# Optimization experiments

Hardware: AMD Instinct MI355X
Metric: run time of the kernel (lower is better)

Reference implementation:

```python
import jax, jax.numpy as jnp
import numpy as np

# Mamba2 config derived from __init__ defaults
D_MODEL, D_STATE, D_CONV, EXPAND, HEADDIM = 768, 16, 4, 2, 64
D_INNER = EXPAND * D_MODEL                      # 1536
NHEADS = D_INNER // HEADDIM                     # 24
NGROUPS = 1
CONV_DIM = D_INNER + 2 * NGROUPS * D_STATE      # 1568
D_IN_PROJ = 2 * D_INNER + 2 * NGROUPS * D_STATE + NHEADS  # 3128
EPS = 1e-5


def setup_inputs() -> dict:
    key = jax.random.key(0)
    ks = jax.random.split(key, 8)
    B, L = 2, 4096
    x = jax.random.normal(ks[0], (B, L, D_MODEL), jnp.float32)
    s_in = 1.0 / np.sqrt(D_MODEL)
    s_out = 1.0 / np.sqrt(D_INNER)
    W_in = jax.random.uniform(ks[1], (D_IN_PROJ, D_MODEL), jnp.float32, -s_in, s_in)
    W_out = jax.random.uniform(ks[2], (D_MODEL, D_INNER), jnp.float32, -s_out, s_out)
    conv_w = jax.random.uniform(ks[3], (CONV_DIM, D_CONV), jnp.float32, -0.5, 0.5)
    conv_b = jax.random.uniform(ks[4], (CONV_DIM,), jnp.float32, -0.5, 0.5)
    # dt init in [1e-3, 0.1] (log-uniform), stored as inverse-softplus bias
    dt = jnp.exp(jax.random.uniform(ks[5], (NHEADS,), jnp.float32) * (np.log(0.1) - np.log(1e-3)) + np.log(1e-3))
    dt_bias = dt + jnp.log(-jnp.expm1(-dt))
    A_log = jnp.log(jax.random.uniform(ks[6], (NHEADS,), jnp.float32, 1.0, 16.0))
    D = jnp.ones((NHEADS,), jnp.float32)
    ln_w = jnp.ones((D_MODEL,), jnp.float32)
    ln_b = jnp.zeros((D_MODEL,), jnp.float32)
    gate_norm_w = jnp.ones((D_INNER,), jnp.float32)
    return dict(x=x, ln_w=ln_w, ln_b=ln_b, W_in=W_in, conv_w=conv_w, conv_b=conv_b,
                dt_bias=dt_bias, A_log=A_log, D=D, gate_norm_w=gate_norm_w, W_out=W_out)


def _layernorm(x, w, b):
    mu = x.mean(-1, keepdims=True)
    var = ((x - mu) ** 2).mean(-1, keepdims=True)
    return (x - mu) * jax.lax.rsqrt(var + EPS) * w + b


def _silu(x):
    return x * jax.nn.sigmoid(x)


def _mamba_block(x, ln_w, ln_b, W_in, conv_w, conv_b, dt_bias, A_log, D, gate_norm_w, W_out):
    Bsz, L, _ = x.shape
    u = _layernorm(x, ln_w, ln_b)
    zxbcdt = jnp.einsum('bld,ed->ble', u, W_in)                 # (b,l,3128)
    z = zxbcdt[..., :D_INNER]
    xBC = zxbcdt[..., D_INNER:D_INNER + CONV_DIM]
    dt = jax.nn.softplus(zxbcdt[..., -NHEADS:] + dt_bias)       # (b,l,h)
    # causal depthwise conv (width D_CONV) + SiLU
    xp = jnp.pad(xBC, ((0, 0), (D_CONV - 1, 0), (0, 0)))
    acc = xp[:, 0:L, :] * conv_w[:, 0]
    for i in range(1, D_CONV):
        acc = acc + xp[:, i:i + L, :] * conv_w[:, i]
    xBC = _silu(acc + conv_b)
    xs = xBC[..., :D_INNER].reshape(Bsz, L, NHEADS, HEADDIM)    # (b,l,h,p)
    Bm = xBC[..., D_INNER:D_INNER + D_STATE]                    # (b,l,n) ngroups=1
    Cm = xBC[..., D_INNER + D_STATE:]                           # (b,l,n)
    A = -jnp.exp(A_log)                                         # (h,)
    dA = jnp.exp(dt * A)                                        # (b,l,h)
    # selective scan: h_t = dA_t * h_{t-1} + dt_t * (x_t outer B_t)
    def step(h, inp):
        dA_t, dt_t, B_t, C_t, x_t = inp                          # (b,h),(b,h),(b,n),(b,n),(b,h,p)
        h = dA_t[..., None, None] * h + jnp.einsum('bh,bn,bhp->bhpn', dt_t, B_t, x_t)
        y = jnp.einsum('bhpn,bn->bhp', h, C_t)
        return h, y
    h0 = jnp.zeros((Bsz, NHEADS, HEADDIM, D_STATE), x.dtype)
    _, ys = jax.lax.scan(step, h0, (dA.transpose(1, 0, 2), dt.transpose(1, 0, 2),
                                    Bm.transpose(1, 0, 2), Cm.transpose(1, 0, 2),
                                    xs.transpose(1, 0, 2, 3)))
    y = ys.transpose(1, 0, 2, 3) + D[:, None] * xs               # (b,l,h,p) skip term
    y = y.reshape(Bsz, L, D_INNER)
    # gated RMSNorm: norm(y * silu(z)) * weight
    g = y * _silu(z)
    g = g * jax.lax.rsqrt((g * g).mean(-1, keepdims=True) + EPS) * gate_norm_w
    out = jnp.einsum('ble,de->bld', g, W_out)
    return x + out


def reference(x, ln_w, ln_b, W_in, conv_w, conv_b, dt_bias, A_log, D, gate_norm_w, W_out):
    return _mamba_block(x, ln_w, ln_b, W_in, conv_w, conv_b, dt_bias, A_log, D, gate_norm_w, W_out)
```

## Files before the change

### kernel.cpp

```cpp
#include <hip/hip_runtime.h>
#include <hip/hip_bf16.h>
#include <stdint.h>

#define SEQ      4096
#define BATCH    2
#define NTOK     (BATCH*SEQ)
#define DMODEL   768
#define DINNER   1536
#define NHEADS   24
#define HEADDIM  64
#define DSTATE   16
#define NPAD     3200
#define EPSV     1e-5f
#define CHUNK    64
#define NCHUNK   (SEQ/CHUNK)
#define SUB      32

typedef __bf16 bf16x8 __attribute__((ext_vector_type(8)));
typedef float  floatx4 __attribute__((ext_vector_type(4)));

__device__ __forceinline__ unsigned short f2bf(float f) {
    union { float f; uint32_t u; } v; v.f = f;
    uint32_t u = v.u;
    uint32_t r = (u + 0x7fffu + ((u >> 16) & 1u)) >> 16;
    return (unsigned short)r;
}

__device__ __forceinline__ float bf2f(unsigned short h) {
    union { uint32_t u; float f; } v; v.u = (uint32_t)h << 16;
    return v.f;
}

__device__ __forceinline__ float bfl(uint32_t u) {
    union { uint32_t u; float f; } v; v.u = u << 16; return v.f;
}
__device__ __forceinline__ float bfh(uint32_t u) {
    union { uint32_t u; float f; } v; v.u = u & 0xffff0000u; return v.f;
}
__device__ __forceinline__ uint32_t packbf(float lo, float hi) {
    return (uint32_t)f2bf(lo) | ((uint32_t)f2bf(hi) << 16);
}

__device__ __forceinline__ float siluf(float x) { return x / (1.f + __expf(-x)); }

__device__ __forceinline__ void async_cp16(const void* g, void* l) {
    __builtin_amdgcn_global_load_lds(
        (const __attribute__((address_space(1))) void*)g,
        (__attribute__((address_space(3))) void*)l,
        16, 0, 0);
}

__global__ __launch_bounds__(256) void cvt_kernel(
    const float* __restrict__ Win, const float* __restrict__ Wout,
    unsigned short* __restrict__ win16, unsigned short* __restrict__ wout16)
{
    int idx = blockIdx.x * 256 + threadIdx.x;
    const int n1 = NPAD * DMODEL;
    if (idx < n1) {
        int r = idx / DMODEL;
        win16[idx] = (r < 3128) ? f2bf(Win[idx]) : (unsigned short)0;
    } else {
        int i2 = idx - n1;
        if (i2 < DMODEL * DINNER) wout16[i2] = f2bf(Wout[i2]);
    }
}

__global__ __launch_bounds__(256) void ln_kernel(
    const float* __restrict__ x, const float* __restrict__ lnw, const float* __restrict__ lnb,
    unsigned short* __restrict__ u16)
{
    int wave = threadIdx.x >> 6, lane = threadIdx.x & 63;
    int token = blockIdx.x * 4 + wave;
    const float* row = x + (size_t)token * DMODEL;
    float4 v[3];
    float s = 0.f, ss = 0.f;
#pragma unroll
    for (int j = 0; j < 3; ++j) {
        v[j] = *(const float4*)(row + lane*4 + j*256);
        s  += v[j].x + v[j].y + v[j].z + v[j].w;
        ss += v[j].x*v[j].x + v[j].y*v[j].y + v[j].z*v[j].z + v[j].w*v[j].w;
    }
#pragma unroll
    for (int o = 32; o > 0; o >>= 1) { s += __shfl_xor(s, o, 64); ss += __shfl_xor(ss, o, 64); }
    float mean = s * (1.f/768.f);
    float var  = ss * (1.f/768.f) - mean*mean;
    float rstd = rsqrtf(var + EPSV);
    unsigned short* brow = u16 + (size_t)token * DMODEL;
#pragma unroll
    for (int j = 0; j < 3; ++j) {
        int cidx = lane*4 + j*256;
        float4 w4 = *(const float4*)(lnw + cidx);
        float4 b4 = *(const float4*)(lnb + cidx);
        float a0 = (v[j].x - mean)*rstd*w4.x + b4.x;
        float a1 = (v[j].y - mean)*rstd*w4.y + b4.y;
        float a2 = (v[j].z - mean)*rstd*w4.z + b4.z;
        float a3 = (v[j].w - mean)*rstd*w4.w + b4.w;
        ushort4 p; p.x = f2bf(a0); p.y = f2bf(a1); p.z = f2bf(a2); p.w = f2bf(a3);
        *(ushort4*)(brow + cidx) = p;
    }
}

__global__ __launch_bounds__(256) void dt_kernel(
    const float* __restrict__ raw24, const float* __restrict__ dt_bias,
    const float* __restrict__ A_log, float* __restrict__ dtT, float* __restrict__ dAT)
{
    int tid = blockIdx.x * 256 + threadIdx.x;
    int h   = tid >> 13;
    int tok = tid & (NTOK-1);
    float raw = raw24[(size_t)tok*NHEADS + h] + dt_bias[h];
    float dt = (raw > 20.f) ? raw : log1pf(__expf(raw));
    float A = -__expf(A_log[h]);
    dtT[tid] = dt;
    dAT[tid] = __expf(dt * A);
}

__global__ __launch_bounds__(256, 3) void gemm1_kernel(
    const unsigned short* __restrict__ A, const unsigned short* __restrict__ Bt,
    unsigned short* __restrict__ z16, unsigned short* __restrict__ x16,
    float* __restrict__ bcr, float* __restrict__ raw24)
{
    constexpr int K = DMODEL;
    __shared__ unsigned short As[128*64];
    __shared__ unsigned short Bs[128*64];
    const int tid  = threadIdx.x;
    const int lane = tid & 63;
    const int wave = tid >> 6;
    const int id   = blockIdx.x;
    const int xcd  = id & 7;
    const int j5   = id >> 3;
    const int m0 = (xcd*8 + (j5 & 7)) * 128;
    const int n0 = (j5 >> 3) * 128;
    const int wm = (wave & 1) * 64;
    const int wn = (wave >> 1) * 64;

    floatx4 acc[4][4];
#pragma unroll
    for (int i = 0; i < 4; ++i)
#pragma unroll
        for (int j = 0; j < 4; ++j) acc[i][j] = floatx4{0.f, 0.f, 0.f, 0.f};

    const int srow8  = lane >> 3;
    const int schunk = lane & 7;
    const int sscol  = (schunk ^ srow8) * 8;

    for (int k0 = 0; k0 < K; k0 += 64) {
        __syncthreads();
#pragma unroll
        for (int o = 0; o < 4; ++o) {
            int row = wave*32 + o*8 + srow8;
            async_cp16(A + (size_t)(m0 + row) * K + k0 + sscol, As + row*64 + schunk*8);
        }
#pragma unroll
        for (int o = 0; o < 4; ++o) {
            int row = wave*32 + o*8 + srow8;
            async_cp16(Bt + (size_t)(n0 + row) * K + k0 + sscol, Bs + row*64 + schunk*8);
        }
        __syncthreads();
        const int fr  = lane & 15;
        const int q8  = lane >> 4;
        const int key = fr & 7;
#pragma unroll
        for (int ks = 0; ks < 2; ++ks) {
            const int ch = ((ks*4 + q8) ^ key) * 8;
            bf16x8 a[4], b[4];
#pragma unroll
            for (int i = 0; i < 4; ++i)
                a[i] = *(const bf16x8*)(As + (wm + i*16 + fr)*64 + ch);
#pragma unroll
            for (int j = 0; j < 4; ++j)
                b[j] = *(const bf16x8*)(Bs + (wn + j*16 + fr)*64 + ch);
#pragma unroll
            for (int i = 0; i < 4; ++i)
#pragma unroll
                for (int j = 0; j < 4; ++j)
                    acc[i][j] = __builtin_amdgcn_mfma_f32_16x16x32_bf16(a[i], b[j], acc[i][j], 0, 0, 0);
        }
    }

    const int col = lane & 15;
    const int rq  = (lane >> 4) * 4;
    if (n0 < DINNER) {
#pragma unroll
        for (int i = 0; i < 4; ++i)
#pragma unroll
            for (int j = 0; j < 4; ++j)
#pragma unroll
                for (int r = 0; r < 4; ++r) {
                    int gm = m0 + wm + i*16 + rq + r;
                    int gn = n0 + wn + j*16 + col;
                    z16[(size_t)gm * DINNER + gn] = f2bf(acc[i][j][r]);
                }
    } else if (n0 < 3072) {
#pragma unroll
        for (int i = 0; i < 4; ++i)
#pragma unroll
            for (int j = 0; j < 4; ++j)
#pragma unroll
                for (int r = 0; r < 4; ++r) {
                    int gm = m0 + wm + i*16 + rq + r;
                    int gn = n0 + wn + j*16 + col;
                    x16[(size_t)gm * DINNER + (gn - DINNER)] = f2bf(acc[i][j][r]);
                }
    } else {
#pragma unroll
        for (int i = 0; i < 4; ++i)
#pragma unroll
            for (int j = 0; j < 4; ++j)
#pragma unroll
                for (int r = 0; r < 4; ++r) {
                    int gm = m0 + wm + i*16 + rq + r;
                    int gn = n0 + wn + j*16 + col;
                    if (gn < 3104)
                        bcr[(size_t)gm * 32 + (gn - 3072)] = acc[i][j][r];
                    else if (gn < 3128)
                        raw24[(size_t)gm * NHEADS + (gn - 3104)] = acc[i][j][r];
                }
    }
}

__global__ __launch_bounds__(256, 4) void gemm2_kernel(
    const unsigned short* __restrict__ A, const unsigned short* __restrict__ Bt,
    float* __restrict__ Cf, const float* __restrict__ resid)
{
    constexpr int K = DINNER;
    __shared__ unsigned short As[64*64];
    __shared__ unsigned short Bs[128*64];
    const int tid  = threadIdx.x;
    const int lane = tid & 63;
    const int wave = tid >> 6;
    const int id   = blockIdx.x;
    const int xcd  = id & 7;
    const int j6   = id >> 3;
    const int m0 = (xcd*16 + j6/6) * 64;
    const int n0 = (j6 % 6) * 128;
    const int wm = (wave & 1) * 32;
    const int wn = (wave >> 1) * 64;

    floatx4 acc[2][4];
#pragma unroll
    for (int i = 0; i < 2; ++i)
#pragma unroll
        for (int j = 0; j < 4; ++j) acc[i][j] = floatx4{0.f, 0.f, 0.f, 0.f};

    const int srow8  = lane >> 3;
    const int schunk = lane & 7;
    const int sscol  = (schunk ^ srow8) * 8;

    for (int k0 = 0; k0 < K; k0 += 64) {
        __syncthreads();
#pragma unroll
        for (int o = 0; o < 2; ++o) {
            int row = wave*16 + o*8 + srow8;
            async_cp16(A + (size_t)(m0 + row) * K + k0 + sscol, As + row*64 + schunk*8);
        }
#pragma unroll
        for (int o = 0; o < 4; ++o) {
            int row = wave*32 + o*8 + srow8;
            async_cp16(Bt + (size_t)(n0 + row) * K + k0 + sscol, Bs + row*64 + schunk*8);
        }
        __syncthreads();
        const int fr  = lane & 15;
        const int q8  = lane >> 4;
        const int key = fr & 7;
#pragma unroll
        for (int ks = 0; ks < 2; ++ks) {
            const int ch = ((ks*4 + q8) ^ key) * 8;
            bf16x8 a[2], b[4];
#pragma unroll
            for (int i = 0; i < 2; ++i)
                a[i] = *(const bf16x8*)(As + (wm + i*16 + fr)*64 + ch);
#pragma unroll
            for (int j = 0; j < 4; ++j)
                b[j] = *(const bf16x8*)(Bs + (wn + j*16 + fr)*64 + ch);
#pragma unroll
            for (int i = 0; i < 2; ++i)
#pragma unroll
                for (int j = 0; j < 4; ++j)
                    acc[i][j] = __builtin_amdgcn_mfma_f32_16x16x32_bf16(a[i], b[j], acc[i][j], 0, 0, 0);
        }
    }

    const int col = lane & 15;
    const int rq  = (lane >> 4) * 4;
#pragma unroll
    for (int i = 0; i < 2; ++i)
#pragma unroll
        for (int j = 0; j < 4; ++j)
#pragma unroll
            for (int r = 0; r < 4; ++r) {
                int gm = m0 + wm + i*16 + rq + r;
                int gn = n0 + wn + j*16 + col;
                Cf[(size_t)gm * DMODEL + gn] = acc[i][j][r] + resid[(size_t)gm * DMODEL + gn];
            }
}

__global__ __launch_bounds__(256) void scan_pass1(
    const unsigned short* __restrict__ x16, const float* __restrict__ bcr,
    const float* __restrict__ dAT, const float* __restrict__ dtT,
    const float* __restrict__ cw, const float* __restrict__ cb, const float* __restrict__ Dp,
    float* __restrict__ hloc, float* __restrict__ pprod, unsigned short* __restrict__ ylocal16)
{
    int wave = threadIdx.x >> 6, lane = threadIdx.x & 63;
    int blk = blockIdx.x * 4 + wave;
    int c = blk & (NCHUNK-1), bh = blk >> 6;
    int h = bh % NHEADS, b = bh / NHEADS;
    int row0 = b * SEQ + c * CHUNK;
    int l0 = c * CHUNK;
    int tb = h * NTOK + row0;
    __shared__ float bcraw[4][35][32];
    __shared__ float bcsc[4][32][32];
    __shared__ float av[4][32], dv[4][32];

    const int cx = h*64 + lane;
    float cwx0 = cw[cx*4+0], cwx1 = cw[cx*4+1], cwx2 = cw[cx*4+2], cwx3 = cw[cx*4+3];
    float cbx = cb[cx];
    const int nBC = lane & 31;
    float cwc0 = cw[(DINNER+nBC)*4+0], cwc1 = cw[(DINNER+nBC)*4+1];
    float cwc2 = cw[(DINNER+nBC)*4+2], cwc3 = cw[(DINNER+nBC)*4+3];
    float cbc = cb[DINNER+nBC];
    float Dh = Dp[h];

    float xm3 = (l0 >= 3) ? bf2f(x16[(size_t)(row0-3)*DINNER + cx]) : 0.f;
    float xm2 = (l0 >= 2) ? bf2f(x16[(size_t)(row0-2)*DINNER + cx]) : 0.f;
    float xm1 = (l0 >= 1) ? bf2f(x16[(size_t)(row0-1)*DINNER + cx]) : 0.f;

    float hst[16];
#pragma unroll
    for (int n = 0; n < 16; ++n) hst[n] = 0.f;
    float aprod = 1.f;

    for (int sc = 0; sc < CHUNK/SUB; ++sc) {
        int rb = row0 + sc * SUB;
        int lb = l0 + sc * SUB;
        __syncthreads();
#pragma unroll
        for (int it = 0; it < 5; ++it) {
            int idx = it*64 + lane;
            if (idx < 280) {
                int s = idx >> 3, q = idx & 7;
                float4 val = {0.f,0.f,0.f,0.f};
                if (lb - 3 + s >= 0)
                    val = *(const float4*)(bcr + (size_t)(rb-3+s)*32 + q*4);
                *(float4*)&bcraw[wave][s][q*4] = val;
            }
        }
        if (lane < 32) av[wave][lane] = dAT[(size_t)tb + sc*SUB + lane];
        else           dv[wave][lane-32] = dtT[(size_t)tb + sc*SUB + lane - 32];
        float xr[SUB];
#pragma unroll
        for (int s = 0; s < SUB; ++s)
            xr[s] = bf2f(x16[(size_t)(rb+s)*DINNER + cx]);
        __syncthreads();
#pragma unroll
        for (int it = 0; it < 16; ++it) {
            int s = it*2 + (lane >> 5);
            float v = cbc + bcraw[wave][s][nBC]*cwc0 + bcraw[wave][s+1][nBC]*cwc1
                          + bcraw[wave][s+2][nBC]*cwc2 + bcraw[wave][s+3][nBC]*cwc3;
            bcsc[wave][s][nBC] = siluf(v);
        }
        __syncthreads();
#pragma unroll 2
        for (int s = 0; s < SUB; ++s) {
            float a = av[wave][s];
            float xc = siluf(cbx + xm3*cwx0 + xm2*cwx1 + xm1*cwx2 + xr[s]*cwx3);
            xm3 = xm2; xm2 = xm1; xm1 = xr[s];
            float scale = dv[wave][s] * xc;
            float y = Dh * xc;
            const float4* bp4 = (const float4*)&bcsc[wave][s][0];
            float4 bv[8];
#pragma unroll
            for (int q = 0; q < 8; ++q) bv[q] = bp4[q];
            const float* bp = (const float*)bv;
#pragma unroll
            for (int n = 0; n < 16; ++n) hst[n] = a*hst[n] + scale*bp[n];
#pragma unroll
            for (int n = 0; n < 16; ++n) y += hst[n] * bp[16+n];
            aprod *= a;
            ylocal16[(size_t)(rb+s)*DINNER + cx] = f2bf(y);
        }
    }
    float* o = hloc + (size_t)blk * 1024 + lane * 16;
#pragma unroll
    for (int n = 0; n < 16; ++n) o[n] = hst[n];
    if (lane == 0) pprod[blk] = aprod;
}

__global__ __launch_bounds__(256) void scan_pass2(
    const float* __restrict__ hloc, const float* __restrict__ pprod, float* __restrict__ hstart)
{
    __shared__ float sm[64*256];
    __shared__ float pp[64];
    const int tid = threadIdx.x;
    const int bh  = blockIdx.x >> 2;
    const int q   = blockIdx.x & 3;
    const float* src = hloc + (size_t)bh * 65536 + q * 256;
#pragma unroll
    for (int it = 0; it < 16; ++it) {
        int idx = it*256 + tid;
        int c   = idx >> 6;
        int e4  = (idx & 63) * 4;
        *(float4*)&sm[c*256 + e4] = *(const float4*)(src + (size_t)c*1024 + e4);
    }
    if (tid < 64) pp[tid] = pprod[bh*64 + tid];
    __syncthreads();
    float h = 0.f;
    float* dst = hstart + (size_t)bh * 65536 + q * 256 + tid;
#pragma unroll 8
    for (int c = 0; c < 64; ++c) {
        dst[(size_t)c * 1024] = h;
        h = pp[c] * h + sm[c*256 + tid];
    }
}

__global__ __launch_bounds__(256) void scan_pass3(
    const float* __restrict__ bcr, const float* __restrict__ dAT,
    const float* __restrict__ cw, const float* __restrict__ cb,
    const float* __restrict__ hstart, unsigned short* __restrict__ ylocal16)
{
    int wave = threadIdx.x >> 6, lane = threadIdx.x & 63;
    int blk = blockIdx.x * 4 + wave;
    int c = blk & (NCHUNK-1), bh = blk >> 6;
    int h = bh % NHEADS, b = bh / NHEADS;
    int row0 = b * SEQ + c * CHUNK;
    int l0 = c * CHUNK;
    int tb = h * NTOK + row0;
    __shared__ float craw[4][35][16];
    __shared__ float csc[4][32][16];
    __shared__ float av[4][32];

    const int cx = h*64 + lane;
    const int nC = lane & 15;
    float cwc0 = cw[(DINNER+16+nC)*4+0], cwc1 = cw[(DINNER+16+nC)*4+1];
    float cwc2 = cw[(DINNER+16+nC)*4+2], cwc3 = cw[(DINNER+16+nC)*4+3];
    float cbc = cb[DINNER+16+nC];

    float h0[16];
    const float* hs = hstart + (size_t)blk * 1024 + lane * 16;
#pragma unroll
    for (int n = 0; n < 16; ++n) h0[n] = hs[n];
    float cd = 1.f;

    for (int sc = 0; sc < CHUNK/SUB; ++sc) {
        int rb = row0 + sc * SUB;
        int lb = l0 + sc * SUB;
        __syncthreads();
#pragma unroll
        for (int it = 0; it < 3; ++it) {
            int idx = it*64 + lane;
            if (idx < 140) {
                int s = idx >> 2, q = idx & 3;
                float4 val = {0.f,0.f,0.f,0.f};
                if (lb - 3 + s >= 0)
                    val = *(const float4*)(bcr + (size_t)(rb-3+s)*32 + 16 + q*4);
                *(float4*)&craw[wave][s][q*4] = val;
            }
        }
        if (lane < 32) av[wave][lane] = dAT[(size_t)tb + sc*SUB + lane];
        float yr[SUB];
#pragma unroll
        for (int s = 0; s < SUB; ++s)
            yr[s] = bf2f(ylocal16[(size_t)(rb+s)*DINNER + cx]);
        __syncthreads();
#pragma unroll
        for (int it = 0; it < 8; ++it) {
            int s = it*4 + (lane >> 4);
            float v = cbc + craw[wave][s][nC]*cwc0 + craw[wave][s+1][nC]*cwc1
                          + craw[wave][s+2][nC]*cwc2 + craw[wave][s+3][nC]*cwc3;
            csc[wave][s][nC] = siluf(v);
        }
        __syncthreads();
#pragma unroll 2
        for (int s = 0; s < SUB; ++s) {
            cd *= av[wave][s];
            const float4* cp4 = (const float4*)&csc[wave][s][0];
            float4 cv[4];
#pragma unroll
            for (int q = 0; q < 4; ++q) cv[q] = cp4[q];
            const float* cp = (const float*)cv;
            float corr = 0.f;
#pragma unroll
            for (int n = 0; n < 16; ++n) corr += cp[n] * h0[n];
            ylocal16[(size_t)(rb+s)*DINNER + cx] = f2bf(yr[s] + cd * corr);
        }
    }
}

__global__ __launch_bounds__(256) void gate_kernel(
    const unsigned short* __restrict__ yv16, const unsigned short* __restrict__ z16,
    const float* __restrict__ gw, unsigned short* __restrict__ g16)
{
    int wave = threadIdx.x >> 6, lane = threadIdx.x & 63;
    int token = blockIdx.x * 4 + wave;
    const uint4* yrow = (const uint4*)(yv16 + (size_t)token * DINNER);
    const uint4* zrow = (const uint4*)(z16 + (size_t)token * DINNER);
    float g[3][8];
    float ss = 0.f;
#pragma unroll
    for (int j = 0; j < 3; ++j) {
        uint4 y8 = yrow[lane + j*64];
        uint4 z8 = zrow[lane + j*64];
        const uint32_t* yp = (const uint32_t*)&y8;
        const uint32_t* zp = (const uint32_t*)&z8;
#pragma unroll
        for (int q = 0; q < 4; ++q) {
            float a = bfl(yp[q]) * siluf(bfl(zp[q]));
            float bvl = bfh(yp[q]) * siluf(bfh(zp[q]));
            g[j][q*2]   = a;
            g[j][q*2+1] = bvl;
            ss += a*a + bvl*bvl;
        }
    }
#pragma unroll
    for (int o = 32; o > 0; o >>= 1) ss += __shfl_xor(ss, o, 64);
    float scale = rsqrtf(ss * (1.f/1536.f) + EPSV);
    uint4* orow = (uint4*)(g16 + (size_t)token * DINNER);
#pragma unroll
    for (int j = 0; j < 3; ++j) {
        int ebase = (lane + j*64) * 8;
        float4 w0 = *(const float4*)(gw + ebase);
        float4 w1 = *(const float4*)(gw + ebase + 4);
        uint4 p;
        p.x = packbf(g[j][0]*scale*w0.x, g[j][1]*scale*w0.y);
        p.y = packbf(g[j][2]*scale*w0.z, g[j][3]*scale*w0.w);
        p.z = packbf(g[j][4]*scale*w1.x, g[j][5]*scale*w1.y);
        p.w = packbf(g[j][6]*scale*w1.z, g[j][7]*scale*w1.w);
        orow[lane + j*64] = p;
    }
}

extern "C" void kernel_launch(void* const* d_in, const int* in_sizes, int n_in,
                              void* d_out, int out_size, void* d_ws, size_t ws_size,
                              hipStream_t stream)
{
    const float* x        = (const float*)d_in[0];
    const float* ln_w     = (const float*)d_in[1];
    const float* ln_b     = (const float*)d_in[2];
    const float* W_in     = (const float*)d_in[3];
    const float* conv_w   = (const float*)d_in[4];
    const float* conv_b   = (const float*)d_in[5];
    const float* dt_bias  = (const float*)d_in[6];
    const float* A_log    = (const float*)d_in[7];
    const float* Dp       = (const float*)d_in[8];
    const float* gate_w   = (const float*)d_in[9];
    const float* W_out    = (const float*)d_in[10];
    float* out = (float*)d_out;

    char* ws = (char*)d_ws;
    size_t off = 0;
    auto alloc = [&](size_t bytes) -> void* {
        void* p = ws + off;
        off += (bytes + 255) & ~(size_t)255;
        return p;
    };
    unsigned short* u16    = (unsigned short*)alloc((size_t)NTOK*DMODEL*2);
    unsigned short* win16  = (unsigned short*)alloc((size_t)NPAD*DMODEL*2);
    float*          dtT    = (float*)alloc((size_t)NTOK*NHEADS*4);
    float*          dAT    = (float*)alloc((size_t)NTOK*NHEADS*4);
    float*          raw24  = (float*)alloc((size_t)NTOK*NHEADS*4);
    unsigned short* x16    = (unsigned short*)alloc((size_t)NTOK*DINNER*2);
    float*          bcr    = (float*)alloc((size_t)NTOK*32*4);
    unsigned short* wout16 = (unsigned short*)alloc((size_t)DMODEL*DINNER*2);
    unsigned short* z16    = (unsigned short*)alloc((size_t)NTOK*DINNER*2);
    unsigned short* y16    = (unsigned short*)alloc((size_t)NTOK*DINNER*2);
    unsigned short* g16    = (unsigned short*)alloc((size_t)NTOK*DINNER*2);
    float*          pprod  = (float*)alloc((size_t)BATCH*NHEADS*NCHUNK*4);
    float* hloc   = (float*)u16;
    float* hstart = (float*)g16;

    cvt_kernel<<<(NPAD*DMODEL + DMODEL*DINNER)/256, 256, 0, stream>>>(W_in, W_out, win16, wout16);
    ln_kernel<<<NTOK/4, 256, 0, stream>>>(x, ln_w, ln_b, u16);
    gemm1_kernel<<<1600, 256, 0, stream>>>(u16, win16, z16, x16, bcr, raw24);
    dt_kernel<<<NTOK*NHEADS/256, 256, 0, stream>>>(raw24, dt_bias, A_log, dtT, dAT);
    scan_pass1<<<BATCH*NHEADS*NCHUNK/4, 256, 0, stream>>>(x16, bcr, dAT, dtT, conv_w, conv_b, Dp, hloc, pprod, y16);
    scan_pass2<<<BATCH*NHEADS*4, 256, 0, stream>>>(hloc, pprod, hstart);
    scan_pass3<<<BATCH*NHEADS*NCHUNK/4, 256, 0, stream>>>(bcr, dAT, conv_w, conv_b, hstart, y16);
    gate_kernel<<<NTOK/4, 256, 0, stream>>>(y16, z16, gate_w, g16);
    gemm2_kernel<<<768, 256, 0, stream>>>(g16, wout16, out, x);
}
```

Measured before the change: 261.8 us.

## Fuse LN with weight conversion, fold dt into GEMM1 epilogue, enlarge GEMM2 tile

Merges the layernorm and weight-conversion kernels into one prep launch and vectorizes the fp32-to-bf16 conversion to four elements per thread. Moves the softplus/exp dt computation into the GEMM1 epilogue, which removes the raw24 buffer and a separate kernel. Switches GEMM2 from 64x128 to 128x128 tiles with 384 blocks. This cuts launches and memory round trips. The trade-off is lower occupancy and fewer blocks in GEMM2, plus strided transposed stores from the GEMM1 epilogue.

```diff
diff --git a/kernel.cpp b/kernel.cpp
--- a/kernel.cpp
+++ b/kernel.cpp
@@ -15,6 +15,7 @@
 #define CHUNK    64
 #define NCHUNK   (SEQ/CHUNK)
 #define SUB      32
+#define LNBLK    2048
 
 typedef __bf16 bf16x8 __attribute__((ext_vector_type(8)));
 typedef float  floatx4 __attribute__((ext_vector_type(4)));
@@ -50,74 +51,70 @@
         16, 0, 0);
 }
 
-__global__ __launch_bounds__(256) void cvt_kernel(
+__global__ __launch_bounds__(256) void prep_kernel(
+    const float* __restrict__ x, const float* __restrict__ lnw, const float* __restrict__ lnb,
+    unsigned short* __restrict__ u16,
     const float* __restrict__ Win, const float* __restrict__ Wout,
     unsigned short* __restrict__ win16, unsigned short* __restrict__ wout16)
 {
-    int idx = blockIdx.x * 256 + threadIdx.x;
-    const int n1 = NPAD * DMODEL;
-    if (idx < n1) {
-        int r = idx / DMODEL;
-        win16[idx] = (r < 3128) ? f2bf(Win[idx]) : (unsigned short)0;
+    if (blockIdx.x < LNBLK) {
+        int wave = threadIdx.x >> 6, lane = threadIdx.x & 63;
+        int token = blockIdx.x * 4 + wave;
+        const float* row = x + (size_t)token * DMODEL;
+        float4 v[3];
+        float s = 0.f, ss = 0.f;
+#pragma unroll
+        for (int j = 0; j < 3; ++j) {
+            v[j] = *(const float4*)(row + lane*4 + j*256);
+            s  += v[j].x + v[j].y + v[j].z + v[j].w;
+            ss += v[j].x*v[j].x + v[j].y*v[j].y + v[j].z*v[j].z + v[j].w*v[j].w;
+        }
+#pragma unroll
+        for (int o = 32; o > 0; o >>= 1) { s += __shfl_xor(s, o, 64); ss += __shfl_xor(ss, o, 64); }
+        float mean = s * (1.f/768.f);
+        float var  = ss * (1.f/768.f) - mean*mean;
+        float rstd = rsqrtf(var + EPSV);
+        unsigned short* brow = u16 + (size_t)token * DMODEL;
+#pragma unroll
+        for (int j = 0; j < 3; ++j) {
+            int cidx = lane*4 + j*256;
+            float4 w4 = *(const float4*)(lnw + cidx);
+            float4 b4 = *(const float4*)(lnb + cidx);
+            float a0 = (v[j].x - mean)*rstd*w4.x + b4.x;
+            float a1 = (v[j].y - mean)*rstd*w4.y + b4.y;
+            float a2 = (v[j].z - mean)*rstd*w4.z + b4.z;
+            float a3 = (v[j].w - mean)*rstd*w4.w + b4.w;
+            ushort4 p; p.x = f2bf(a0); p.y = f2bf(a1); p.z = f2bf(a2); p.w = f2bf(a3);
+            *(ushort4*)(brow + cidx) = p;
+        }
     } else {
-        int i2 = idx - n1;
-        if (i2 < DMODEL * DINNER) wout16[i2] = f2bf(Wout[i2]);
-    }
-}
-
-__global__ __launch_bounds__(256) void ln_kernel(
-    const float* __restrict__ x, const float* __restrict__ lnw, const float* __restrict__ lnb,
-    unsigned short* __restrict__ u16)
-{
-    int wave = threadIdx.x >> 6, lane = threadIdx.x & 63;
-    int token = blockIdx.x * 4 + wave;
-    const float* row = x + (size_t)token * DMODEL;
-    float4 v[3];
-    float s = 0.f, ss = 0.f;
-#pragma unroll
-    for (int j = 0; j < 3; ++j) {
-        v[j] = *(const float4*)(row + lane*4 + j*256);
-        s  += v[j].x + v[j].y + v[j].z + v[j].w;
-        ss += v[j].x*v[j].x + v[j].y*v[j].y + v[j].z*v[j].z + v[j].w*v[j].w;
-    }
-#pragma unroll
-    for (int o = 32; o > 0; o >>= 1) { s += __shfl_xor(s, o, 64); ss += __shfl_xor(ss, o, 64); }
-    float mean = s * (1.f/768.f);
-    float var  = ss * (1.f/768.f) - mean*mean;
-    float rstd = rsqrtf(var + EPSV);
-    unsigned short* brow = u16 + (size_t)token * DMODEL;
-#pragma unroll
-    for (int j = 0; j < 3; ++j) {
-        int cidx = lane*4 + j*256;
-        float4 w4 = *(const float4*)(lnw + cidx);
-        float4 b4 = *(const float4*)(lnb + cidx);
-        float a0 = (v[j].x - mean)*rstd*w4.x + b4.x;
-        float a1 = (v[j].y - mean)*rstd*w4.y + b4.y;
-        float a2 = (v[j].z - mean)*rstd*w4.z + b4.z;
-        float a3 = (v[j].w - mean)*rstd*w4.w + b4.w;
-        ushort4 p; p.x = f2bf(a0); p.y = f2bf(a1); p.z = f2bf(a2); p.w = f2bf(a3);
-        *(ushort4*)(brow + cidx) = p;
-    }
-}
-
-__global__ __launch_bounds__(256) void dt_kernel(
-    const float* __restrict__ raw24, const float* __restrict__ dt_bias,
-    const float* __restrict__ A_log, float* __restrict__ dtT, float* __restrict__ dAT)
-{
-    int tid = blockIdx.x * 256 + threadIdx.x;
-    int h   = tid >> 13;
-    int tok = tid & (NTOK-1);
-    float raw = raw24[(size_t)tok*NHEADS + h] + dt_bias[h];
-    float dt = (raw > 20.f) ? raw : log1pf(__expf(raw));
-    float A = -__expf(A_log[h]);
-    dtT[tid] = dt;
-    dAT[tid] = __expf(dt * A);
+        int e = ((blockIdx.x - LNBLK) * 256 + threadIdx.x) * 4;
+        const int n1 = NPAD * DMODEL;
+        if (e < n1) {
+            int r = e / DMODEL;
+            ushort4 p = {0, 0, 0, 0};
+            if (r < 3128) {
+                float4 v = *(const float4*)(Win + e);
+                p.x = f2bf(v.x); p.y = f2bf(v.y); p.z = f2bf(v.z); p.w = f2bf(v.w);
+            }
+            *(ushort4*)(win16 + e) = p;
+        } else {
+            int e2 = e - n1;
+            if (e2 < DMODEL * DINNER) {
+                float4 v = *(const float4*)(Wout + e2);
+                ushort4 p; p.x = f2bf(v.x); p.y = f2bf(v.y); p.z = f2bf(v.z); p.w = f2bf(v.w);
+                *(ushort4*)(wout16 + e2) = p;
+            }
+        }
+    }
 }
 
 __global__ __launch_bounds__(256, 3) void gemm1_kernel(
     const unsigned short* __restrict__ A, const unsigned short* __restrict__ Bt,
     unsigned short* __restrict__ z16, unsigned short* __restrict__ x16,
-    float* __restrict__ bcr, float* __restrict__ raw24)
+    float* __restrict__ bcr,
+    const float* __restrict__ dt_bias, const float* __restrict__ A_log,
+    float* __restrict__ dtT, float* __restrict__ dAT)
 {
     constexpr int K = DMODEL;
     __shared__ unsigned short As[128*64];
@@ -212,18 +209,24 @@
                     int gn = n0 + wn + j*16 + col;
                     if (gn < 3104)
                         bcr[(size_t)gm * 32 + (gn - 3072)] = acc[i][j][r];
-                    else if (gn < 3128)
-                        raw24[(size_t)gm * NHEADS + (gn - 3104)] = acc[i][j][r];
+                    else if (gn < 3128) {
+                        int h = gn - 3104;
+                        float raw = acc[i][j][r] + dt_bias[h];
+                        float dt = (raw > 20.f) ? raw : log1pf(__expf(raw));
+                        float dA = __expf(dt * -__expf(A_log[h]));
+                        dtT[(size_t)h * NTOK + gm] = dt;
+                        dAT[(size_t)h * NTOK + gm] = dA;
+                    }
                 }
     }
 }
 
-__global__ __launch_bounds__(256, 4) void gemm2_kernel(
+__global__ __launch_bounds__(256, 3) void gemm2_kernel(
     const unsigned short* __restrict__ A, const unsigned short* __restrict__ Bt,
     float* __restrict__ Cf, const float* __restrict__ resid)
 {
     constexpr int K = DINNER;
-    __shared__ unsigned short As[64*64];
+    __shared__ unsigned short As[128*64];
     __shared__ unsigned short Bs[128*64];
     const int tid  = threadIdx.x;
     const int lane = tid & 63;
@@ -231,14 +234,14 @@
     const int id   = blockIdx.x;
     const int xcd  = id & 7;
     const int j6   = id >> 3;
-    const int m0 = (xcd*16 + j6/6) * 64;
-    const int n0 = (j6 % 6) * 128;
-    const int wm = (wave & 1) * 32;
+    const int m0 = (xcd*8 + (j6 & 7)) * 128;
+    const int n0 = (j6 >> 3) * 128;
+    const int wm = (wave & 1) * 64;
     const int wn = (wave >> 1) * 64;
 
-    floatx4 acc[2][4];
-#pragma unroll
-    for (int i = 0; i < 2; ++i)
+    floatx4 acc[4][4];
+#pragma unroll
+    for (int i = 0; i < 4; ++i)
 #pragma unroll
         for (int j = 0; j < 4; ++j) acc[i][j] = floatx4{0.f, 0.f, 0.f, 0.f};
 
@@ -249,8 +252,8 @@
     for (int k0 = 0; k0 < K; k0 += 64) {
         __syncthreads();
 #pragma unroll
-        for (int o = 0; o < 2; ++o) {
-            int row = wave*16 + o*8 + srow8;
+        for (int o = 0; o < 4; ++o) {
+            int row = wave*32 + o*8 + srow8;
             async_cp16(A + (size_t)(m0 + row) * K + k0 + sscol, As + row*64 + schunk*8);
         }
 #pragma unroll
@@ -265,15 +268,15 @@
 #pragma unroll
         for (int ks = 0; ks < 2; ++ks) {
             const int ch = ((ks*4 + q8) ^ key) * 8;
-            bf16x8 a[2], b[4];
-#pragma unroll
-            for (int i = 0; i < 2; ++i)
+            bf16x8 a[4], b[4];
+#pragma unroll
+            for (int i = 0; i < 4; ++i)
                 a[i] = *(const bf16x8*)(As + (wm + i*16 + fr)*64 + ch);
 #pragma unroll
             for (int j = 0; j < 4; ++j)
                 b[j] = *(const bf16x8*)(Bs + (wn + j*16 + fr)*64 + ch);
 #pragma unroll
-            for (int i = 0; i < 2; ++i)
+            for (int i = 0; i < 4; ++i)
 #pragma unroll
                 for (int j = 0; j < 4; ++j)
                     acc[i][j] = __builtin_amdgcn_mfma_f32_16x16x32_bf16(a[i], b[j], acc[i][j], 0, 0, 0);
@@ -283,7 +286,7 @@
     const int col = lane & 15;
     const int rq  = (lane >> 4) * 4;
 #pragma unroll
-    for (int i = 0; i < 2; ++i)
+    for (int i = 0; i < 4; ++i)
 #pragma unroll
         for (int j = 0; j < 4; ++j)
 #pragma unroll
@@ -556,7 +559,6 @@
     unsigned short* win16  = (unsigned short*)alloc((size_t)NPAD*DMODEL*2);
     float*          dtT    = (float*)alloc((size_t)NTOK*NHEADS*4);
     float*          dAT    = (float*)alloc((size_t)NTOK*NHEADS*4);
-    float*          raw24  = (float*)alloc((size_t)NTOK*NHEADS*4);
     unsigned short* x16    = (unsigned short*)alloc((size_t)NTOK*DINNER*2);
     float*          bcr    = (float*)alloc((size_t)NTOK*32*4);
     unsigned short* wout16 = (unsigned short*)alloc((size_t)DMODEL*DINNER*2);
@@ -567,13 +569,12 @@
     float* hloc   = (float*)u16;
     float* hstart = (float*)g16;
 
-    cvt_kernel<<<(NPAD*DMODEL + DMODEL*DINNER)/256, 256, 0, stream>>>(W_in, W_out, win16, wout16);
-    ln_kernel<<<NTOK/4, 256, 0, stream>>>(x, ln_w, ln_b, u16);
-    gemm1_kernel<<<1600, 256, 0, stream>>>(u16, win16, z16, x16, bcr, raw24);
-    dt_kernel<<<NTOK*NHEADS/256, 256, 0, stream>>>(raw24, dt_bias, A_log, dtT, dAT);
+    prep_kernel<<<LNBLK + (NPAD*DMODEL + DMODEL*DINNER)/1024, 256, 0, stream>>>(
+        x, ln_w, ln_b, u16, W_in, W_out, win16, wout16);
+    gemm1_kernel<<<1600, 256, 0, stream>>>(u16, win16, z16, x16, bcr, dt_bias, A_log, dtT, dAT);
     scan_pass1<<<BATCH*NHEADS*NCHUNK/4, 256, 0, stream>>>(x16, bcr, dAT, dtT, conv_w, conv_b, Dp, hloc, pprod, y16);
     scan_pass2<<<BATCH*NHEADS*4, 256, 0, stream>>>(hloc, pprod, hstart);
     scan_pass3<<<BATCH*NHEADS*NCHUNK/4, 256, 0, stream>>>(bcr, dAT, conv_w, conv_b, hstart, y16);
     gate_kernel<<<NTOK/4, 256, 0, stream>>>(y16, z16, gate_w, g16);
-    gemm2_kernel<<<768, 256, 0, stream>>>(g16, wout16, out, x);
-}
+    gemm2_kernel<<<384, 256, 0, stream>>>(g16, wout16, out, x);
+}
```

New measurement: 282.6 us. 1.08x slower.
